# Optimization experiments

Hardware: AMD Instinct MI355X
Metric: run time of the kernel (lower is better)

## Reference

```python
import jax, jax.numpy as jnp
import numpy as np

B, S, D_MODEL, H, N_LAYERS = 4, 1024, 512, 8, 6
DEPTH = D_MODEL // H


def setup_inputs() -> dict:
    key = jax.random.key(0)
    ks = jax.random.split(key, 16)
    sc = 1.0 / np.sqrt(D_MODEL)
    inp = {
        'v': jax.random.normal(ks[0], (B, S, D_MODEL), jnp.float32),
        'q': jax.random.normal(ks[1], (B, S, D_MODEL), jnp.float32),
        'k': jax.random.normal(ks[2], (B, S, D_MODEL), jnp.float32),
        'wq_w': jax.random.normal(ks[3], (D_MODEL, D_MODEL), jnp.float32) * sc,
        'wq_b': jnp.zeros((D_MODEL,), jnp.float32),
        'wk_w': jax.random.normal(ks[4], (D_MODEL, D_MODEL), jnp.float32) * sc,
        'wk_b': jnp.zeros((D_MODEL,), jnp.float32),
        'wv_w': jax.random.normal(ks[5], (D_MODEL, D_MODEL), jnp.float32) * sc,
        'wv_b': jnp.zeros((D_MODEL,), jnp.float32),
        'wo_w': jax.random.normal(ks[6], (D_MODEL, D_MODEL), jnp.float32) * sc,
        'wo_b': jnp.zeros((D_MODEL,), jnp.float32),
        'aug_hb': jax.random.uniform(ks[7], (N_LAYERS, 1), jnp.float32),
        'aug_pi': jax.random.uniform(ks[8], (N_LAYERS, 1), jnp.float32),
        'aug_at': jax.random.uniform(ks[9], (N_LAYERS, 1), jnp.float32),
        'table_hb': jax.random.normal(ks[10], (S, S), jnp.float32),
        'table_pi': jax.random.normal(ks[11], (S, S), jnp.float32),
        'mask': (jax.random.uniform(ks[12], (B, 1, S, S)) < 0.1).astype(jnp.float32),
        'block_num': 0,
    }
    return inp


def _split_heads(x):
    # (B, S, d_model) -> (B, H, S, depth)
    return x.reshape(B, S, H, DEPTH).transpose(0, 2, 1, 3)


def reference(v, q, k, wq_w, wq_b, wk_w, wk_b, wv_w, wv_b, wo_w, wo_b,
              aug_hb, aug_pi, aug_at, table_hb, table_pi, mask, block_num):
    qh = _split_heads(q @ wq_w + wq_b)
    kh = _split_heads(k @ wk_w + wk_b)
    vh = _split_heads(v @ wv_w + wv_b)

    # NOTE: original call site swaps q/k positionally, so scores = K . Q^T
    scores = jnp.einsum('bhid,bhjd->bhij', kh, qh)  # (B,H,S,S)
    dk = jnp.float32(DEPTH)
    logits = scores / jnp.sqrt(dk) + mask * (-1e9)

    # per-layer table augmentation (tables broadcast over batch & heads)
    logits = logits * aug_at[block_num] \
        + aug_hb[block_num] * table_hb \
        + aug_pi[block_num] * table_pi

    # joint softmax over axes (2, 3)
    m = jnp.max(logits, axis=(2, 3), keepdims=True)
    e = jnp.exp(logits - m)
    attn = e / jnp.sum(e, axis=(2, 3), keepdims=True)

    ctx = jnp.einsum('bhij,bhjd->bhid', attn, vh)          # (B,H,S,depth)
    ctx = ctx.transpose(0, 2, 1, 3).reshape(B, S, D_MODEL)  # concat heads
    out = ctx @ wo_w + wo_b
    return out, attn
```

## Files before the change

### kernel.cpp

```cpp
#include <hip/hip_runtime.h>
#include <math.h>

#define NS 1024
#define DM 512
#define NH 8
#define DEPTH 64

#define OFF_QH   0
#define OFF_KH   2097152
#define OFF_VH   4194304
#define OFF_CTX0 0
#define OFF_CTX1 2097152
#define OFF_PART 6291456

#define ESW(row, col) ((col) ^ ((((row) >> 3) & 7) << 2))

#define LO_SCALE 2048.0f
#define LO_INV   (1.0f/2048.0f)
#define F16_MIN_NORM 6.1035156e-5f
#define ASCALE   4096.0f
#define AUNSCALE (1.0f/4096.0f)

typedef float f4 __attribute__((ext_vector_type(4)));
typedef _Float16 h8 __attribute__((ext_vector_type(8)));
typedef float f32x4v __attribute__((ext_vector_type(4)));

#define SPLIT1(x, hi_e, lo_e) {                                          \
    const float x_ = (x);                                                \
    _Float16 t = (fabsf(x_) >= F16_MIN_NORM) ? (_Float16)x_ : (_Float16)0.f; \
    hi_e = t;                                                            \
    lo_e = (_Float16)((x_ - (float)t) * LO_SCALE);                       \
}

#define SPLIT8(u0, u1, hi, lo) {                                         \
    SPLIT1(u0.x, hi[0], lo[0]) SPLIT1(u0.y, hi[1], lo[1])                \
    SPLIT1(u0.z, hi[2], lo[2]) SPLIT1(u0.w, hi[3], lo[3])                \
    SPLIT1(u1.x, hi[4], lo[4]) SPLIT1(u1.y, hi[5], lo[5])                \
    SPLIT1(u1.z, hi[6], lo[6]) SPLIT1(u1.w, hi[7], lo[7])                \
}

#define MM(accH, accM, a_h, a_l, b_h, b_l) {                                   \
    accH = __builtin_amdgcn_mfma_f32_16x16x32_f16(a_h, b_h, accH, 0, 0, 0);    \
    accM = __builtin_amdgcn_mfma_f32_16x16x32_f16(a_l, b_h, accM, 0, 0, 0);    \
    accM = __builtin_amdgcn_mfma_f32_16x16x32_f16(a_h, b_l, accM, 0, 0, 0);    \
}
#define MM1(acc, a_h, a_l, b_h, b_l) {                                         \
    acc = __builtin_amdgcn_mfma_f32_16x16x32_f16(a_h, b_h, acc, 0, 0, 0);      \
    acc = __builtin_amdgcn_mfma_f32_16x16x32_f16(a_l, b_h, acc, 0, 0, 0);      \
    acc = __builtin_amdgcn_mfma_f32_16x16x32_f16(a_h, b_l, acc, 0, 0, 0);      \
}

__device__ __forceinline__ void prep_one(
    const float* __restrict__ W, _Float16* __restrict__ whi,
    _Float16* __restrict__ wlo, int g)
{
    const int kk = g >> 7;
    const int n  = (g & 127) * 4;
    const float4 f = *(const float4*)(W + (size_t)kk * DM + n);
    const int gbase = (kk >> 3) * 128 + (kk & 7);
    #define PREP1(val, nn) {                                             \
        const int a_ = ((nn) >> 4) * 8192 + gbase + ((nn) & 15) * 8;     \
        _Float16 h_; _Float16 l_;                                        \
        SPLIT1(val, h_, l_)                                              \
        whi[a_] = h_; wlo[a_] = l_;                                      \
    }
    PREP1(f.x, n + 0) PREP1(f.y, n + 1) PREP1(f.z, n + 2) PREP1(f.w, n + 3)
    #undef PREP1
}

__global__ __launch_bounds__(256) void k_prep_qkv(
    const float* __restrict__ wq, const float* __restrict__ wk,
    const float* __restrict__ wv, float* __restrict__ attn)
{
    const int w = blockIdx.y;
    const float* W = (w == 0) ? wq : (w == 1) ? wk : wv;
    _Float16* base = (_Float16*)attn + (size_t)w * 524288;
    prep_one(W, base, base + 262144, blockIdx.x * 256 + threadIdx.x);
}

__global__ __launch_bounds__(256) void k_prep_wo(
    const float* __restrict__ wo, float* __restrict__ ws)
{
    _Float16* base = (_Float16*)(ws + OFF_VH);
    prep_one(wo, base, base + 262144, blockIdx.x * 256 + threadIdx.x);
}

__global__ __launch_bounds__(256, 3) void k_proj(
    const float* __restrict__ q, const float* __restrict__ k, const float* __restrict__ v,
    const float* __restrict__ bq, const float* __restrict__ bk, const float* __restrict__ bv,
    float* __restrict__ ws, const float* __restrict__ attn)
{
    const float *X, *bias; int wsel;
    if (blockIdx.z == 0)      { X=q; bias=bq; wsel=0; }
    else if (blockIdx.z == 1) { X=k; bias=bk; wsel=1; }
    else                      { X=v; bias=bv; wsel=2; }
    float* outf = ws + OFF_VH;
    _Float16* outh = (_Float16*)(ws + (wsel == 0 ? OFF_QH : OFF_KH));

    const int f = blockIdx.x + (blockIdx.y << 3);
    const int n0 = (f >> 5) * 64, m0 = (f & 31) * 128;
    const int tid = threadIdx.x, l = tid & 63, w = tid >> 6;
    const int lr = l & 15, lg = l >> 4;

    const _Float16* whi = (const _Float16*)attn + (size_t)wsel * 524288;
    const _Float16* wlo = whi + 262144;
    const float* ap0 = X + (size_t)(m0 + w*32 + lr) * DM + lg*8;
    const float* ap1 = ap0 + (size_t)16 * DM;
    const _Float16* bh_base = whi + (size_t)(n0 >> 4) * 8192 + lg*128 + lr*8;
    const _Float16* bl_base = wlo + (size_t)(n0 >> 4) * 8192 + lg*128 + lr*8;

    f32x4v aH00 = 0, aH01 = 0, aH02 = 0, aH03 = 0;
    f32x4v aH10 = 0, aH11 = 0, aH12 = 0, aH13 = 0;
    f32x4v aM00 = 0, aM01 = 0, aM02 = 0, aM03 = 0;
    f32x4v aM10 = 0, aM11 = 0, aM12 = 0, aM13 = 0;

    #pragma unroll 1
    for (int kb = 0; kb < DM; kb += 32) {
        h8 ah0, al0, ah1, al1;
        {
            const float4 u0 = *(const float4*)(ap0 + kb);
            const float4 u1 = *(const float4*)(ap0 + kb + 4);
            SPLIT8(u0, u1, ah0, al0);
            const float4 v0 = *(const float4*)(ap1 + kb);
            const float4 v1 = *(const float4*)(ap1 + kb + 4);
            SPLIT8(v0, v1, ah1, al1);
        }
        const int boff = kb * 16;
        const h8 bh0 = *(const h8*)(bh_base + boff);
        const h8 bh1 = *(const h8*)(bh_base + boff + 8192);
        const h8 bh2 = *(const h8*)(bh_base + boff + 16384);
        const h8 bh3 = *(const h8*)(bh_base + boff + 24576);
        const h8 bl0 = *(const h8*)(bl_base + boff);
        const h8 bl1 = *(const h8*)(bl_base + boff + 8192);
        const h8 bl2 = *(const h8*)(bl_base + boff + 16384);
        const h8 bl3 = *(const h8*)(bl_base + boff + 24576);

        MM(aH00, aM00, ah0, al0, bh0, bl0) MM(aH01, aM01, ah0, al0, bh1, bl1)
        MM(aH02, aM02, ah0, al0, bh2, bl2) MM(aH03, aM03, ah0, al0, bh3, bl3)
        MM(aH10, aM10, ah1, al1, bh0, bl0) MM(aH11, aM11, ah1, al1, bh1, bl1)
        MM(aH12, aM12, ah1, al1, bh2, bl2) MM(aH13, aM13, ah1, al1, bh3, bl3)
    }

    const int h = n0 >> 6;
    #define STORE_TILE(accH, accM, nt, mt) {                                 \
        const int n = n0 + (nt)*16 + lr;                                     \
        const float bsv = bias[n];                                           \
        const int d = n & 63;                                                \
        const int mbase = m0 + w*32 + (mt)*16 + lg*4;                        \
        _Pragma("unroll")                                                    \
        for (int r = 0; r < 4; ++r) {                                        \
            const int m = mbase + r;                                         \
            const int bb = m >> 10, s = m & 1023;                            \
            const float val = fmaf(accM[r], LO_INV, accH[r]) + bsv;          \
            if (wsel == 2) {                                                 \
                outf[(((size_t)(bb*NH + h))*NS + s)*DEPTH + d] = val;        \
            } else {                                                         \
                _Float16* p = outh + (size_t)(bb*NH + h)*131072              \
                                   + (size_t)s*64 + d;                       \
                const _Float16 hi_ = (_Float16)val;                          \
                p[0]     = hi_;                                              \
                p[65536] = (_Float16)(val - (float)hi_);                     \
            }                                                                \
        }                                                                    \
    }
    STORE_TILE(aH00, aM00, 0, 0) STORE_TILE(aH10, aM10, 0, 1)
    STORE_TILE(aH01, aM01, 1, 0) STORE_TILE(aH11, aM11, 1, 1)
    STORE_TILE(aH02, aM02, 2, 0) STORE_TILE(aH12, aM12, 2, 1)
    STORE_TILE(aH03, aM03, 3, 0) STORE_TILE(aH13, aM13, 3, 1)
    #undef STORE_TILE
}

__global__ __launch_bounds__(256, 3) void k_score(
    float* __restrict__ ws,
    const float* __restrict__ t_hb, const float* __restrict__ t_pi,
    const float* __restrict__ mask,
    const float* __restrict__ aug_hb, const float* __restrict__ aug_pi,
    const float* __restrict__ aug_at, const int* __restrict__ bnum,
    float* __restrict__ attn)
{
    __shared__ float wred[4];
    const int bh = blockIdx.z, b = bh >> 3;
    const int f = blockIdx.x + (blockIdx.y << 3);
    const int r = f & 7, qq = f >> 3;
    const int it = ((r & 1) << 2) | (qq & 3);
    const int jt_ = ((r >> 1) << 1) | (qq >> 2);
    const int i0 = it * 128, j0 = jt_ * 128;
    const _Float16* kb_ = (const _Float16*)(ws + OFF_KH) + (size_t)bh * 131072;
    const _Float16* qb_ = (const _Float16*)(ws + OFF_QH) + (size_t)bh * 131072;
    const int tid = threadIdx.x, l = tid & 63, w = tid >> 6;
    const int lr = l & 15, lg = l >> 4;

    const _Float16* ka = kb_ + (size_t)(i0 + w*32 + lr) * 64 + lg*8;
    const _Float16* qa = qb_ + (size_t)(j0 + lr) * 64 + lg*8;

    f32x4v acc[2][8] = {};
    #pragma unroll
    for (int d0 = 0; d0 < 2; ++d0) {
        const int dd = d0 * 32;
        const h8 ah0 = *(const h8*)(ka + dd);
        const h8 al0 = *(const h8*)(ka + dd + 65536);
        const h8 ah1 = *(const h8*)(ka + dd + 16*64);
        const h8 al1 = *(const h8*)(ka + dd + 16*64 + 65536);
        #pragma unroll
        for (int jt = 0; jt < 8; ++jt) {
            const h8 bhf = *(const h8*)(qa + dd + jt*16*64);
            const h8 blf = *(const h8*)(qa + dd + jt*16*64 + 65536);
            MM1(acc[0][jt], ah0, al0, bhf, blf)
            MM1(acc[1][jt], ah1, al1, bhf, blf)
        }
    }

    const int bn = bnum[0];
    const float at = aug_at[bn], hb = aug_hb[bn], pi = aug_pi[bn];
    const float sc_at = 0.125f*at, m_at = -1e9f*at;
    float local = 0.f;
    #pragma unroll
    for (int it2 = 0; it2 < 2; ++it2) {
        #pragma unroll
        for (int rr = 0; rr < 4; ++rr) {
            const int gi = i0 + w*32 + it2*16 + lg*4 + rr;
            const size_t mrow = ((size_t)b*NS + gi)*NS;
            const size_t trow = (size_t)gi*NS;
            const size_t arow = ((size_t)bh*NS + gi)*NS;
            #pragma unroll
            for (int jt = 0; jt < 8; ++jt) {
                const int gj = j0 + jt*16 + lr;
                const float mv = mask[mrow + gj];
                const float th = t_hb[trow + gj];
                const float tp = t_pi[trow + gj];
                const float e = __expf(fmaf(acc[it2][jt][rr], sc_at,
                                       fmaf(mv, m_at, fmaf(hb, th, pi*tp))));
                __builtin_nontemporal_store(e, attn + arow + gj);
                local += e;
            }
        }
    }
    #pragma unroll
    for (int o = 32; o > 0; o >>= 1) local += __shfl_down(local, o);
    if ((tid & 63) == 0) wred[tid >> 6] = local;
    __syncthreads();
    if (tid == 0)
        ws[OFF_PART + bh*64 + it*8 + jt_] =
            (wred[0] + wred[1]) + (wred[2] + wred[3]);
}

__global__ __launch_bounds__(256, 4) void k_pv(
    float* __restrict__ ws, float* __restrict__ attn)
{
    __shared__ float Es[64][68];
    __shared__ float Vs[64][68];
    __shared__ float s_inv;
    const int F = blockIdx.x + (blockIdx.y << 1) + (blockIdx.z << 5);
    const int r = F & 7, s = F >> 3;
    const int bh = (r << 2) | (s & 3);
    const int w = s >> 2;
    const int i0 = (w >> 1) * 64;
    const int jh = w & 1;
    const int b = bh >> 3, h = bh & 7;
    const float* vh = ws + OFF_VH + (size_t)bh*NS*DEPTH;
    float* pctx = ws + (jh ? OFF_CTX1 : OFF_CTX0);
    const int tid = threadIdx.x, tx = tid & 15, ty = tid >> 4;
    const int er_ = tid >> 4, ec4 = tid & 15;

    if (tid < 64) {
        float vsum = ws[OFF_PART + bh*64 + tid];
        #pragma unroll
        for (int o = 32; o > 0; o >>= 1) vsum += __shfl_down(vsum, o);
        if (tid == 0) s_inv = 1.0f / vsum;
    }
    __syncthreads();
    const float inv = s_inv;

    float acc[4][4] = {};
    for (int jt = 0; jt < 8; ++jt) {
        const int j0 = jh*512 + jt*64;
        #pragma unroll
        for (int l = 0; l < 4; ++l) {
            const int rr = er_ + l*16;
            float* ap = attn + ((size_t)bh*NS + i0 + rr)*NS + j0 + ec4*4;
            f4 e4 = __builtin_nontemporal_load((const f4*)ap);
            e4 *= inv;
            __builtin_nontemporal_store(e4, (f4*)ap);
            Es[ec4*4+0][ESW(ec4*4+0, rr)] = e4.x;
            Es[ec4*4+1][ESW(ec4*4+1, rr)] = e4.y;
            Es[ec4*4+2][ESW(ec4*4+2, rr)] = e4.z;
            Es[ec4*4+3][ESW(ec4*4+3, rr)] = e4.w;
            *(float4*)&Vs[rr][ec4*4] = *(const float4*)(vh + (size_t)(j0+rr)*DEPTH + ec4*4);
        }
        __syncthreads();
        #pragma unroll
        for (int jj = 0; jj < 64; ++jj) {
            const float4 a  = *(const float4*)&Es[jj][ESW(jj, ty*4)];
            const float4 vv = *(const float4*)&Vs[jj][tx*4];
            const float av[4] = {a.x,a.y,a.z,a.w};
            const float vw[4] = {vv.x,vv.y,vv.z,vv.w};
            #pragma unroll
            for (int i = 0; i < 4; ++i)
                #pragma unroll
                for (int d = 0; d < 4; ++d)
                    acc[i][d] = fmaf(av[i], vw[d], acc[i][d]);
        }
        __syncthreads();
    }
    #pragma unroll
    for (int i = 0; i < 4; ++i) {
        const int gi = i0 + ty*4 + i;
        float4 o;
        o.x = acc[i][0]; o.y = acc[i][1]; o.z = acc[i][2]; o.w = acc[i][3];
        *(float4*)(pctx + ((size_t)b*NS + gi)*DM + h*DEPTH + tx*4) = o;
    }
}

__global__ __launch_bounds__(256, 3) void k_out(
    const float* __restrict__ wsc, const float* __restrict__ bo,
    float* __restrict__ outp)
{
    const int f = blockIdx.x + (blockIdx.y << 3);
    const int n0 = (f >> 5) * 64, m0 = (f & 31) * 128;
    const int tid = threadIdx.x, l = tid & 63, w = tid >> 6;
    const int lr = l & 15, lg = l >> 4;

    const _Float16* whi = (const _Float16*)(wsc + OFF_VH);
    const _Float16* wlo = whi + 262144;
    const float* ap0 = wsc + OFF_CTX0 + (size_t)(m0 + w*32 + lr) * DM + lg*8;
    const float* ap1 = wsc + OFF_CTX1 + (size_t)(m0 + w*32 + lr) * DM + lg*8;
    const _Float16* bh_base = whi + (size_t)(n0 >> 4) * 8192 + lg*128 + lr*8;
    const _Float16* bl_base = wlo + (size_t)(n0 >> 4) * 8192 + lg*128 + lr*8;

    f32x4v aH00 = 0, aH01 = 0, aH02 = 0, aH03 = 0;
    f32x4v aH10 = 0, aH11 = 0, aH12 = 0, aH13 = 0;
    f32x4v aM00 = 0, aM01 = 0, aM02 = 0, aM03 = 0;
    f32x4v aM10 = 0, aM11 = 0, aM12 = 0, aM13 = 0;

    #pragma unroll 1
    for (int kb = 0; kb < DM; kb += 32) {
        h8 ah0, al0, ah1, al1;
        {
            float4 u0 = *(const float4*)(ap0 + kb);
            float4 u1 = *(const float4*)(ap0 + kb + 4);
            const float4 c0 = *(const float4*)(ap1 + kb);
            const float4 c1 = *(const float4*)(ap1 + kb + 4);
            u0.x=(u0.x+c0.x)*ASCALE; u0.y=(u0.y+c0.y)*ASCALE;
            u0.z=(u0.z+c0.z)*ASCALE; u0.w=(u0.w+c0.w)*ASCALE;
            u1.x=(u1.x+c1.x)*ASCALE; u1.y=(u1.y+c1.y)*ASCALE;
            u1.z=(u1.z+c1.z)*ASCALE; u1.w=(u1.w+c1.w)*ASCALE;
            SPLIT8(u0, u1, ah0, al0);
            float4 v0 = *(const float4*)(ap0 + (size_t)16*DM + kb);
            float4 v1 = *(const float4*)(ap0 + (size_t)16*DM + kb + 4);
            const float4 d0 = *(const float4*)(ap1 + (size_t)16*DM + kb);
            const float4 d1 = *(const float4*)(ap1 + (size_t)16*DM + kb + 4);
            v0.x=(v0.x+d0.x)*ASCALE; v0.y=(v0.y+d0.y)*ASCALE;
            v0.z=(v0.z+d0.z)*ASCALE; v0.w=(v0.w+d0.w)*ASCALE;
            v1.x=(v1.x+d1.x)*ASCALE; v1.y=(v1.y+d1.y)*ASCALE;
            v1.z=(v1.z+d1.z)*ASCALE; v1.w=(v1.w+d1.w)*ASCALE;
            SPLIT8(v0, v1, ah1, al1);
        }
        const int boff = kb * 16;
        const h8 bh0 = *(const h8*)(bh_base + boff);
        const h8 bh1 = *(const h8*)(bh_base + boff + 8192);
        const h8 bh2 = *(const h8*)(bh_base + boff + 16384);
        const h8 bh3 = *(const h8*)(bh_base + boff + 24576);
        const h8 bl0 = *(const h8*)(bl_base + boff);
        const h8 bl1 = *(const h8*)(bl_base + boff + 8192);
        const h8 bl2 = *(const h8*)(bl_base + boff + 16384);
        const h8 bl3 = *(const h8*)(bl_base + boff + 24576);

        MM(aH00, aM00, ah0, al0, bh0, bl0) MM(aH01, aM01, ah0, al0, bh1, bl1)
        MM(aH02, aM02, ah0, al0, bh2, bl2) MM(aH03, aM03, ah0, al0, bh3, bl3)
        MM(aH10, aM10, ah1, al1, bh0, bl0) MM(aH11, aM11, ah1, al1, bh1, bl1)
        MM(aH12, aM12, ah1, al1, bh2, bl2) MM(aH13, aM13, ah1, al1, bh3, bl3)
    }

    #define STORE_TILE(accH, accM, nt, mt) {                                 \
        const int n = n0 + (nt)*16 + lr;                                     \
        const float bsv = bo[n];                                             \
        const int mbase = m0 + w*32 + (mt)*16 + lg*4;                        \
        _Pragma("unroll")                                                    \
        for (int r = 0; r < 4; ++r)                                          \
            outp[(size_t)(mbase + r)*DM + n] =                               \
                fmaf(accM[r], LO_INV, accH[r]) * AUNSCALE + bsv;             \
    }
    STORE_TILE(aH00, aM00, 0, 0) STORE_TILE(aH10, aM10, 0, 1)
    STORE_TILE(aH01, aM01, 1, 0) STORE_TILE(aH11, aM11, 1, 1)
    STORE_TILE(aH02, aM02, 2, 0) STORE_TILE(aH12, aM12, 2, 1)
    STORE_TILE(aH03, aM03, 3, 0) STORE_TILE(aH13, aM13, 3, 1)
    #undef STORE_TILE
}

extern "C" void kernel_launch(void* const* d_in, const int* in_sizes, int n_in,
                              void* d_out, int out_size, void* d_ws, size_t ws_size,
                              hipStream_t stream)
{
    const float* v    = (const float*)d_in[0];
    const float* q    = (const float*)d_in[1];
    const float* k    = (const float*)d_in[2];
    const float* wq_w = (const float*)d_in[3];
    const float* wq_b = (const float*)d_in[4];
    const float* wk_w = (const float*)d_in[5];
    const float* wk_b = (const float*)d_in[6];
    const float* wv_w = (const float*)d_in[7];
    const float* wv_b = (const float*)d_in[8];
    const float* wo_w = (const float*)d_in[9];
    const float* wo_b = (const float*)d_in[10];
    const float* aug_hb = (const float*)d_in[11];
    const float* aug_pi = (const float*)d_in[12];
    const float* aug_at = (const float*)d_in[13];
    const float* t_hb   = (const float*)d_in[14];
    const float* t_pi   = (const float*)d_in[15];
    const float* mask   = (const float*)d_in[16];
    const int*   bnum   = (const int*)d_in[17];

    float* ws   = (float*)d_ws;
    float* outp = (float*)d_out;
    float* attn = (float*)d_out + (size_t)4*NS*DM;

    hipLaunchKernelGGL(k_prep_qkv, dim3(256, 3), dim3(256), 0, stream,
                       wq_w, wk_w, wv_w, attn);
    hipLaunchKernelGGL(k_proj, dim3(8, 32, 3), dim3(256), 0, stream,
                       q, k, v, wq_b, wk_b, wv_b, ws, attn);
    hipLaunchKernelGGL(k_score, dim3(8, 8, 32), dim3(256), 0, stream,
                       ws, t_hb, t_pi, mask, aug_hb, aug_pi, aug_at, bnum, attn);
    hipLaunchKernelGGL(k_pv, dim3(2, 16, 32), dim3(256), 0, stream, ws, attn);
    hipLaunchKernelGGL(k_prep_wo, dim3(256, 1), dim3(256), 0, stream, wo_w, ws);
    hipLaunchKernelGGL(k_out, dim3(8, 32), dim3(256), 0, stream,
                       ws, wo_b, outp);
}
```

Baseline: 242.9 us.

## Precombine mask and tables into fp16 bias buffer; use cached attn stores

Adds a pre-pass kernel that folds the mask, both tables and the per-layer scalars into one fp16 additive bias per (batch, i, j). It stores this in the unused output buffer, so the score kernel reads one 2-byte value instead of three fp32 values per element, repeated across the 8 heads. The score and PV kernels also switch attn stores and loads from nontemporal to regular, so the L2/MALL cache can keep attn between kernels. The cost is an extra pass over the 16MB mask and reduced precision of the bias term in fp16, with a clamp at -60000.

```diff
diff --git a/kernel.cpp b/kernel.cpp
--- a/kernel.cpp
+++ b/kernel.cpp
@@ -23,6 +23,7 @@
 
 typedef float f4 __attribute__((ext_vector_type(4)));
 typedef _Float16 h8 __attribute__((ext_vector_type(8)));
+typedef _Float16 h4 __attribute__((ext_vector_type(4)));
 typedef float f32x4v __attribute__((ext_vector_type(4)));
 
 #define SPLIT1(x, hi_e, lo_e) {                                          \
@@ -83,6 +84,31 @@
 {
     _Float16* base = (_Float16*)(ws + OFF_VH);
     prep_one(wo, base, base + 262144, blockIdx.x * 256 + threadIdx.x);
+}
+
+__global__ __launch_bounds__(256) void k_prep_aux(
+    const float* __restrict__ mask, const float* __restrict__ t_hb,
+    const float* __restrict__ t_pi,
+    const float* __restrict__ aug_hb, const float* __restrict__ aug_pi,
+    const float* __restrict__ aug_at, const int* __restrict__ bnum,
+    float* __restrict__ outp)
+{
+    const int g = blockIdx.x * 256 + threadIdx.x;
+    const size_t e0 = (size_t)g * 4;
+    const size_t t0 = e0 & (size_t)(NS*NS - 1);
+    const int bn = bnum[0];
+    const float at = aug_at[bn], hb = aug_hb[bn], pi = aug_pi[bn];
+    const float m_at = -1e9f * at;
+    const f4 m4 = *(const f4*)(mask + e0);
+    const f4 th = *(const f4*)(t_hb + t0);
+    const f4 tp = *(const f4*)(t_pi + t0);
+    h4 o;
+    float a;
+    a = fmaf(m4.x, m_at, fmaf(hb, th.x, pi*tp.x)); if (a < -60000.f) a = -60000.f; o[0] = (_Float16)a;
+    a = fmaf(m4.y, m_at, fmaf(hb, th.y, pi*tp.y)); if (a < -60000.f) a = -60000.f; o[1] = (_Float16)a;
+    a = fmaf(m4.z, m_at, fmaf(hb, th.z, pi*tp.z)); if (a < -60000.f) a = -60000.f; o[2] = (_Float16)a;
+    a = fmaf(m4.w, m_at, fmaf(hb, th.w, pi*tp.w)); if (a < -60000.f) a = -60000.f; o[3] = (_Float16)a;
+    *(h4*)((_Float16*)outp + e0) = o;
 }
 
 __global__ __launch_bounds__(256, 3) void k_proj(
@@ -172,9 +198,7 @@
 
 __global__ __launch_bounds__(256, 3) void k_score(
     float* __restrict__ ws,
-    const float* __restrict__ t_hb, const float* __restrict__ t_pi,
-    const float* __restrict__ mask,
-    const float* __restrict__ aug_hb, const float* __restrict__ aug_pi,
+    const _Float16* __restrict__ aux,
     const float* __restrict__ aug_at, const int* __restrict__ bnum,
     float* __restrict__ attn)
 {
@@ -211,26 +235,21 @@
     }
 
     const int bn = bnum[0];
-    const float at = aug_at[bn], hb = aug_hb[bn], pi = aug_pi[bn];
-    const float sc_at = 0.125f*at, m_at = -1e9f*at;
+    const float sc_at = 0.125f * aug_at[bn];
     float local = 0.f;
     #pragma unroll
     for (int it2 = 0; it2 < 2; ++it2) {
         #pragma unroll
         for (int rr = 0; rr < 4; ++rr) {
             const int gi = i0 + w*32 + it2*16 + lg*4 + rr;
-            const size_t mrow = ((size_t)b*NS + gi)*NS;
-            const size_t trow = (size_t)gi*NS;
+            const size_t xrow = ((size_t)b*NS + gi)*NS;
             const size_t arow = ((size_t)bh*NS + gi)*NS;
             #pragma unroll
             for (int jt = 0; jt < 8; ++jt) {
                 const int gj = j0 + jt*16 + lr;
-                const float mv = mask[mrow + gj];
-                const float th = t_hb[trow + gj];
-                const float tp = t_pi[trow + gj];
-                const float e = __expf(fmaf(acc[it2][jt][rr], sc_at,
-                                       fmaf(mv, m_at, fmaf(hb, th, pi*tp))));
-                __builtin_nontemporal_store(e, attn + arow + gj);
+                const float xv = (float)aux[xrow + gj];
+                const float e = __expf(fmaf(acc[it2][jt][rr], sc_at, xv));
+                attn[arow + gj] = e;
                 local += e;
             }
         }
@@ -278,9 +297,9 @@
         for (int l = 0; l < 4; ++l) {
             const int rr = er_ + l*16;
             float* ap = attn + ((size_t)bh*NS + i0 + rr)*NS + j0 + ec4*4;
-            f4 e4 = __builtin_nontemporal_load((const f4*)ap);
+            f4 e4 = *(const f4*)ap;
             e4 *= inv;
-            __builtin_nontemporal_store(e4, (f4*)ap);
+            *(f4*)ap = e4;
             Es[ec4*4+0][ESW(ec4*4+0, rr)] = e4.x;
             Es[ec4*4+1][ESW(ec4*4+1, rr)] = e4.y;
             Es[ec4*4+2][ESW(ec4*4+2, rr)] = e4.z;
@@ -416,10 +435,12 @@
 
     hipLaunchKernelGGL(k_prep_qkv, dim3(256, 3), dim3(256), 0, stream,
                        wq_w, wk_w, wv_w, attn);
+    hipLaunchKernelGGL(k_prep_aux, dim3(4096), dim3(256), 0, stream,
+                       mask, t_hb, t_pi, aug_hb, aug_pi, aug_at, bnum, outp);
     hipLaunchKernelGGL(k_proj, dim3(8, 32, 3), dim3(256), 0, stream,
                        q, k, v, wq_b, wk_b, wv_b, ws, attn);
     hipLaunchKernelGGL(k_score, dim3(8, 8, 32), dim3(256), 0, stream,
-                       ws, t_hb, t_pi, mask, aug_hb, aug_pi, aug_at, bnum, attn);
+                       ws, (const _Float16*)outp, aug_at, bnum, attn);
     hipLaunchKernelGGL(k_pv, dim3(2, 16, 32), dim3(256), 0, stream, ws, attn);
     hipLaunchKernelGGL(k_prep_wo, dim3(256, 1), dim3(256), 0, stream, wo_w, ws);
     hipLaunchKernelGGL(k_out, dim3(8, 32), dim3(256), 0, stream,
```

Result: faster. 222.8 us (-8.3%).
